# Performance work log

Hardware: AMD Instinct MI355X
Metric: run time of the kernel (lower is better)

The kernel has to match this reference:

```python
import jax, jax.numpy as jnp
import numpy as np

N = 50000      # nodes
E = 800000     # edges (avg degree 16)
F_IN = 256
F_OUT = 128
ALPHA = 0.2    # leaky-relu negative slope


def setup_inputs() -> dict:
    key = jax.random.key(0)
    k1, k2, k3, k4 = jax.random.split(key, 4)
    x = jax.random.normal(k1, (N, F_IN), dtype=jnp.float32)
    # xavier_uniform-like scale for W (gain=1.414)
    limit_w = 1.414 * np.sqrt(6.0 / (F_IN + F_OUT))
    W = jax.random.uniform(k2, (F_IN, F_OUT), dtype=jnp.float32, minval=-limit_w, maxval=limit_w)
    limit_a = 1.414 * np.sqrt(6.0 / (2 * F_OUT + 1))
    a = jax.random.uniform(k3, (2 * F_OUT, 1), dtype=jnp.float32, minval=-limit_a, maxval=limit_a)
    edge = jax.random.randint(k4, (2, E), 0, N)  # edge[0]=row/src, edge[1]=col/dst
    return {"x": x, "W": W, "a": a, "edge": edge}


def reference(x, W, a, edge):
    h = x @ W                                   # [N, F_OUT]
    src, dst = edge[0], edge[1]                 # [E], [E]
    # cat([h_i, h_j], 1) @ a == h_i @ a[:F] + h_j @ a[F:] -> compute per-node halves once
    s_src = h @ a[:F_OUT, 0]                    # [N]
    s_dst = h @ a[F_OUT:, 0]                    # [N]
    e = jax.nn.leaky_relu(s_src[src] + s_dst[dst], negative_slope=ALPHA)  # [E]
    # segment softmax over edges grouped by row (dim=1 softmax of sparse [N,N])
    m = jax.ops.segment_max(e, src, num_segments=N)       # [N], -inf for empty rows
    ex = jnp.exp(e - m[src])                               # [E]
    denom = jax.ops.segment_sum(ex, src, num_segments=N)   # [N]
    attn = ex / denom[src]                                  # [E]
    # sparse mm: h_prime[i] = sum_{edges with row i} attn * h[dst]
    h_prime = jax.ops.segment_sum(attn[:, None] * h[dst], src, num_segments=N)  # [N, F_OUT]
    return jax.nn.elu(h_prime)                  # concat=True path
```

## Files before the change

kernel.cpp:

```cpp
#include <hip/hip_runtime.h>
#include <hip/hip_bf16.h>
#include <math.h>

#define F_IN   256
#define F_OUT  128
#define ALPHA  0.2f
#define TM     64

typedef __attribute__((ext_vector_type(8))) short s16x8;
typedef __attribute__((ext_vector_type(4))) float f32x4;

__device__ __forceinline__ ushort f2bf(float f) {
  __hip_bfloat16 h = __float2bfloat16(f);
  return *reinterpret_cast<ushort*>(&h);
}
__device__ __forceinline__ uint pk2bf(float lo, float hi) {
  return (uint)f2bf(lo) | ((uint)f2bf(hi) << 16);
}
__device__ __forceinline__ float bflo(uint u) { return __uint_as_float(u << 16); }
__device__ __forceinline__ float bfhi(uint u) { return __uint_as_float(u & 0xffff0000u); }

__global__ __launch_bounds__(256) void prep_kernel(
    const float* __restrict__ W, const float* __restrict__ avec,
    ushort* __restrict__ Wf, ushort* __restrict__ Wfs,
    int4* __restrict__ deg4, int n4, int ZB) {
  int b = blockIdx.x;
  if (b < ZB) {
    int i = b * 256 + threadIdx.x;
    if (i < n4) deg4[i] = make_int4(0, 0, 0, 0);
  } else if (b < ZB + 16) {
    int idx = (b - ZB) * 256 + threadIdx.x;
    int kb = idx >> 7, c = idx & 127;
    union { s16x8 v; ushort u[8]; } t;
#pragma unroll
    for (int j = 0; j < 8; ++j) t.u[j] = f2bf(W[(kb * 8 + j) * F_OUT + c]);
    *(s16x8*)&Wf[(size_t)idx * 8] = t.v;
  } else {
    int k = threadIdx.x;
    float s1 = 0.f, s2 = 0.f;
    for (int c = 0; c < F_OUT; ++c) {
      float wv = W[k * F_OUT + c];
      s1 += wv * avec[c];
      s2 += wv * avec[F_OUT + c];
    }
    int kb = k >> 3, j8 = k & 7;
    ushort b1 = f2bf(s1), b2 = f2bf(s2);
#pragma unroll
    for (int cc = 0; cc < 16; ++cc) {
      ushort v = (cc == 0) ? b1 : (cc == 1) ? b2 : (ushort)0;
      Wfs[((size_t)kb * 16 + cc) * 8 + j8] = v;
    }
  }
}

__global__ __launch_bounds__(256) void gemm_hist_kernel(
    const float* __restrict__ X, const ushort* __restrict__ Wf,
    const ushort* __restrict__ Wfs,
    uint* __restrict__ Hb32, float* __restrict__ s_src, float* __restrict__ s_dst,
    int M, int G,
    const int* __restrict__ src, int* __restrict__ deg,
    int* __restrict__ rank, int E) {
  __shared__ __align__(16) char Xs[TM * 256 * 2];
  const int tid = threadIdx.x;

  if (blockIdx.x >= G) {
    int e0 = ((blockIdx.x - G) * 256 + tid) * 4;
    if (e0 + 4 <= E) {
      int4 s4 = *(const int4*)(src + e0);
      int4 r4;
      r4.x = atomicAdd(&deg[s4.x], 1);
      r4.y = atomicAdd(&deg[s4.y], 1);
      r4.z = atomicAdd(&deg[s4.z], 1);
      r4.w = atomicAdd(&deg[s4.w], 1);
      *(int4*)(rank + e0) = r4;
    } else {
      for (int e = e0; e < E; ++e) rank[e] = atomicAdd(&deg[src[e]], 1);
    }
    return;
  }

  const int l = tid & 63;
  const int w = tid >> 6;
  const int lc = l & 15;
  const int lg = l >> 4;
  const int row0 = blockIdx.x * TM;

  s16x8 bfr0[8], bfr1[8];
#pragma unroll
  for (int ks = 0; ks < 8; ++ks) {
    int kb = ks * 4 + lg;
    bfr0[ks] = *(const s16x8*)&Wf[((size_t)kb * F_OUT + w * 16 + lc) * 8];
    bfr1[ks] = *(const s16x8*)&Wf[((size_t)kb * F_OUT + 64 + w * 16 + lc) * 8];
  }

#pragma unroll
  for (int half = 0; half < 2; ++half) {
    f32x4 v[8];
#pragma unroll
    for (int u = 0; u < 4; ++u) {
      int idx = (half * 4 + u) * 256 + tid;
      int r = idx >> 5, kb = idx & 31;
      int gr = row0 + r; gr = (gr < M) ? gr : (M - 1);
      const f32x4* p = (const f32x4*)&X[(size_t)gr * F_IN + kb * 8];
      v[u * 2]     = p[0];
      v[u * 2 + 1] = p[1];
    }
#pragma unroll
    for (int u = 0; u < 4; ++u) {
      int idx = (half * 4 + u) * 256 + tid;
      int r = idx >> 5, kb = idx & 31;
      f32x4 v0 = v[u * 2], v1 = v[u * 2 + 1];
      union { s16x8 vv; ushort uu[8]; } t;
      t.uu[0] = f2bf(v0[0]); t.uu[1] = f2bf(v0[1]); t.uu[2] = f2bf(v0[2]); t.uu[3] = f2bf(v0[3]);
      t.uu[4] = f2bf(v1[0]); t.uu[5] = f2bf(v1[1]); t.uu[6] = f2bf(v1[2]); t.uu[7] = f2bf(v1[3]);
      int byte = ((r >> 4) * 8192) + kb * 256 + (r & 15) * 16;
      byte ^= (kb & 7) << 4;
      *(s16x8*)(Xs + byte) = t.vv;
    }
  }
  __syncthreads();

  f32x4 acc0[4] = {}, acc1[4] = {}, accS[4] = {};
#pragma unroll
  for (int ks = 0; ks < 8; ++ks) {
    int kb = ks * 4 + lg;
    int ab = kb * 256 + lc * 16;
    ab ^= (kb & 7) << 4;
    s16x8 bS;
    if (w == 0) bS = *(const s16x8*)&Wfs[((size_t)kb * 16 + lc) * 8];
#pragma unroll
    for (int rf = 0; rf < 4; ++rf) {
      s16x8 af = *(const s16x8*)(Xs + rf * 8192 + ab);
      acc0[rf] = __builtin_amdgcn_mfma_f32_16x16x32_bf16(af, bfr0[ks], acc0[rf], 0, 0, 0);
      acc1[rf] = __builtin_amdgcn_mfma_f32_16x16x32_bf16(af, bfr1[ks], acc1[rf], 0, 0, 0);
      if (w == 0)
        accS[rf] = __builtin_amdgcn_mfma_f32_16x16x32_bf16(af, bS, accS[rf], 0, 0, 0);
    }
  }

#pragma unroll
  for (int rf = 0; rf < 4; ++rf) {
#pragma unroll
    for (int q = 0; q < 4; ++q) {
      int rg = row0 + rf * 16 + lg * 4 + q;
      if (rg < M)
        Hb32[(size_t)rg * 64 + w * 16 + lc] = pk2bf(acc0[rf][q], acc1[rf][q]);
    }
  }

  if (w == 0 && lc < 2) {
    float* sout = (lc == 0) ? s_src : s_dst;
#pragma unroll
    for (int rf = 0; rf < 4; ++rf) {
#pragma unroll
      for (int q = 0; q < 4; ++q) {
        int rg = row0 + rf * 16 + lg * 4 + q;
        if (rg < M) sout[rg] = accS[rf][q];
      }
    }
  }
}

__global__ void block_sums_kernel(const int* __restrict__ deg, int* __restrict__ bs, int N) {
  int i = blockIdx.x * 256 + threadIdx.x;
  int v = (i < N) ? deg[i] : 0;
  int lane = threadIdx.x & 63, w = threadIdx.x >> 6;
#pragma unroll
  for (int d = 32; d >= 1; d >>= 1) v += __shfl_down(v, d);
  __shared__ int wsum[4];
  if (lane == 0) wsum[w] = v;
  __syncthreads();
  if (threadIdx.x == 0) bs[blockIdx.x] = wsum[0] + wsum[1] + wsum[2] + wsum[3];
}

__global__ void scan_deg_kernel(const int* __restrict__ deg, const int* __restrict__ bs,
                                int* __restrict__ rowptr, int N, int E, int NS) {
  __shared__ int sc[256];
  __shared__ int wsumA[4], wsumB[4];
  int tid = threadIdx.x;
  int lane = tid & 63, w = tid >> 6;

  int bv = (tid < NS) ? bs[tid] : 0;
  int ibv = bv;
#pragma unroll
  for (int d = 1; d < 64; d <<= 1) {
    int t = __shfl_up(ibv, d);
    if (lane >= d) ibv += t;
  }
  if (lane == 63) wsumA[w] = ibv;
  __syncthreads();
  int boff = 0;
  for (int x = 0; x < w; ++x) boff += wsumA[x];
  sc[tid] = boff + ibv - bv;

  int i = blockIdx.x * 256 + tid;
  int v = (i < N) ? deg[i] : 0;
  int iv = v;
#pragma unroll
  for (int d = 1; d < 64; d <<= 1) {
    int t = __shfl_up(iv, d);
    if (lane >= d) iv += t;
  }
  if (lane == 63) wsumB[w] = iv;
  __syncthreads();
  int off = sc[blockIdx.x];
  for (int x = 0; x < w; ++x) off += wsumB[x];
  int excl = off + iv - v;
  if (i < N) rowptr[i] = excl;
  if (i == N - 1) rowptr[N] = E;
}

__global__ __launch_bounds__(256) void scatter_kernel(
    const int* __restrict__ src, const int* __restrict__ dst,
    const int* __restrict__ rank, const int* __restrict__ rowptr,
    int* __restrict__ colidx, int E) {
  int e0 = (blockIdx.x * 256 + threadIdx.x) * 4;
  if (e0 + 4 <= E) {
    int4 s4 = *(const int4*)(src + e0);
    int4 d4 = *(const int4*)(dst + e0);
    int4 r4 = *(const int4*)(rank + e0);
    colidx[rowptr[s4.x] + r4.x] = d4.x;
    colidx[rowptr[s4.y] + r4.y] = d4.y;
    colidx[rowptr[s4.z] + r4.z] = d4.z;
    colidx[rowptr[s4.w] + r4.w] = d4.w;
  } else {
    for (int e = e0; e < E; ++e) colidx[rowptr[src[e]] + rank[e]] = dst[e];
  }
}

__global__ __launch_bounds__(256) void aggregate_kernel(
    const uint* __restrict__ H32, const float* __restrict__ s_src,
    const float* __restrict__ s_dst, const int* __restrict__ rowptr,
    const int* __restrict__ colidx, float* __restrict__ out, int M) {
  int node = blockIdx.x * 4 + (threadIdx.x >> 6);
  int l = threadIdx.x & 63;
  if (node >= M) return;
  const int g = l >> 4;
  const int lc = l & 15;
  int beg = rowptr[node], end = rowptr[node + 1];
  float ssrc = s_src[node];
  float m = -INFINITY, denom = 0.f;
  float acc[8] = {};

  for (int base = beg; base < end; base += 64) {
    int cnt = end - base; if (cnt > 64) cnt = 64;
    int jv = 0; float ev = -INFINITY;
    if (l < cnt) {
      jv = colidx[base + l];
      float e = ssrc + s_dst[jv];
      ev = (e > 0.f) ? e : ALPHA * e;
    }
    float cm = ev;
#pragma unroll
    for (int mask = 1; mask < 64; mask <<= 1) cm = fmaxf(cm, __shfl_xor(cm, mask));
    float mn = fmaxf(m, cm);
    float wv = (l < cnt) ? __expf(ev - mn) : 0.f;
    float sw = wv;
#pragma unroll
    for (int mask = 1; mask < 64; mask <<= 1) sw += __shfl_xor(sw, mask);
    float resc = __expf(m - mn);
    denom = denom * resc + sw;
#pragma unroll
    for (int t = 0; t < 8; ++t) acc[t] *= resc;
    m = mn;

    for (int k = 0; k < cnt; k += 8) {
      int k0 = k + g, k1 = k + 4 + g;
      int j0 = __shfl(jv, k0);
      int j1 = (k1 < 64) ? __shfl(jv, k1) : 0;
      float w0 = __shfl(wv, k0);
      float w1 = (k1 < 64) ? __shfl(wv, k1) : 0.f;
      uint4 u0 = *(const uint4*)(H32 + ((size_t)(uint)j0 << 6) + lc * 4);
      uint4 u1 = *(const uint4*)(H32 + ((size_t)(uint)j1 << 6) + lc * 4);
      acc[0] += w0 * bflo(u0.x) + w1 * bflo(u1.x);
      acc[1] += w0 * bfhi(u0.x) + w1 * bfhi(u1.x);
      acc[2] += w0 * bflo(u0.y) + w1 * bflo(u1.y);
      acc[3] += w0 * bfhi(u0.y) + w1 * bfhi(u1.y);
      acc[4] += w0 * bflo(u0.z) + w1 * bflo(u1.z);
      acc[5] += w0 * bfhi(u0.z) + w1 * bfhi(u1.z);
      acc[6] += w0 * bflo(u0.w) + w1 * bflo(u1.w);
      acc[7] += w0 * bfhi(u0.w) + w1 * bfhi(u1.w);
    }
  }

#pragma unroll
  for (int t = 0; t < 8; ++t) {
    acc[t] += __shfl_xor(acc[t], 16);
    acc[t] += __shfl_xor(acc[t], 32);
  }
  float inv = (denom > 0.f) ? 1.f / denom : 0.f;
  if (g == 0) {
    float4 v;
    v.x = acc[0] * inv; v.y = acc[2] * inv; v.z = acc[4] * inv; v.w = acc[6] * inv;
    v.x = (v.x > 0.f) ? v.x : __expf(v.x) - 1.f;
    v.y = (v.y > 0.f) ? v.y : __expf(v.y) - 1.f;
    v.z = (v.z > 0.f) ? v.z : __expf(v.z) - 1.f;
    v.w = (v.w > 0.f) ? v.w : __expf(v.w) - 1.f;
    *(float4*)&out[(size_t)node * 128 + lc * 4] = v;
  } else if (g == 1) {
    float4 v;
    v.x = acc[1] * inv; v.y = acc[3] * inv; v.z = acc[5] * inv; v.w = acc[7] * inv;
    v.x = (v.x > 0.f) ? v.x : __expf(v.x) - 1.f;
    v.y = (v.y > 0.f) ? v.y : __expf(v.y) - 1.f;
    v.z = (v.z > 0.f) ? v.z : __expf(v.z) - 1.f;
    v.w = (v.w > 0.f) ? v.w : __expf(v.w) - 1.f;
    *(float4*)&out[(size_t)node * 128 + 64 + lc * 4] = v;
  }
}

extern "C" void kernel_launch(void* const* d_in, const int* in_sizes, int n_in,
                              void* d_out, int out_size, void* d_ws, size_t ws_size,
                              hipStream_t stream) {
  const float* x    = (const float*)d_in[0];
  const float* W    = (const float*)d_in[1];
  const float* avec = (const float*)d_in[2];
  const int*   edge = (const int*)d_in[3];

  const int M = in_sizes[0] / F_IN;
  const int E = in_sizes[3] / 2;
  const int* src = edge;
  const int* dst = edge + E;
  float* out = (float*)d_out;

  char* ws = (char*)d_ws;
  uint*   Hb32  = (uint*)ws;   ws += (size_t)M * 64 * sizeof(uint);
  ushort* Wf    = (ushort*)ws; ws += (size_t)32 * F_OUT * 8 * sizeof(ushort);
  ushort* Wfs   = (ushort*)ws; ws += (size_t)32 * 16 * 8 * sizeof(ushort);
  float* s_src  = (float*)ws;  ws += (size_t)M * sizeof(float);
  float* s_dst  = (float*)ws;  ws += (size_t)M * sizeof(float);
  int*   deg    = (int*)ws;    ws += (size_t)M * sizeof(int);
  int*   rowptr = (int*)ws;    ws += (size_t)(M + 1) * sizeof(int);
  int*   rank   = (int*)ws;    ws += (size_t)E * sizeof(int);
  int*   colidx = (int*)ws;    ws += (size_t)E * sizeof(int);
  int*   bsums  = (int*)ws;

  const int NS = (M + 255) / 256;
  const int n4 = M / 4;
  const int ZB = (n4 + 255) / 256;
  const int E4 = (E + 1023) / 1024;
  const int G  = (M + TM - 1) / TM;

  prep_kernel<<<ZB + 17, 256, 0, stream>>>(W, avec, Wf, Wfs, (int4*)deg, n4, ZB);
  gemm_hist_kernel<<<G + E4, 256, 0, stream>>>(x, Wf, Wfs, Hb32, s_src, s_dst,
                                               M, G, src, deg, rank, E);
  block_sums_kernel<<<NS, 256, 0, stream>>>(deg, bsums, M);
  scan_deg_kernel<<<NS, 256, 0, stream>>>(deg, bsums, rowptr, M, E, NS);
  scatter_kernel<<<E4, 256, 0, stream>>>(src, dst, rank, rowptr, colidx, E);
  aggregate_kernel<<<(M + 3) / 4, 256, 0, stream>>>(Hb32, s_src, s_dst, rowptr, colidx, out, M);
}
```

Baseline: 111.7 us.

## Split histogram from GEMM and load X fragments directly into registers

The fused GEMM+histogram launch is split into two kernels, a standalone degree-histogram/rank kernel and a GEMM kernel. The GEMM no longer stages X through LDS with a swizzled layout and a barrier. Each wave now loads its own X rows straight from global memory into MFMA fragment registers and converts them to bf16 inline, and W fragments are loaded per k-step instead of preloaded. This removes LDS traffic and the block barrier, but each of the four waves reloads the same X tile from global/L2 (4x redundant reads) and loses the overlap between the histogram atomics and the GEMM in one grid.

```diff
diff --git a/kernel.cpp b/kernel.cpp
--- a/kernel.cpp
+++ b/kernel.cpp
@@ -53,88 +53,53 @@
   }
 }
 
-__global__ __launch_bounds__(256) void gemm_hist_kernel(
+__global__ __launch_bounds__(256) void gemm_mfma_kernel(
     const float* __restrict__ X, const ushort* __restrict__ Wf,
     const ushort* __restrict__ Wfs,
     uint* __restrict__ Hb32, float* __restrict__ s_src, float* __restrict__ s_dst,
-    int M, int G,
-    const int* __restrict__ src, int* __restrict__ deg,
-    int* __restrict__ rank, int E) {
-  __shared__ __align__(16) char Xs[TM * 256 * 2];
+    int M) {
   const int tid = threadIdx.x;
-
-  if (blockIdx.x >= G) {
-    int e0 = ((blockIdx.x - G) * 256 + tid) * 4;
-    if (e0 + 4 <= E) {
-      int4 s4 = *(const int4*)(src + e0);
-      int4 r4;
-      r4.x = atomicAdd(&deg[s4.x], 1);
-      r4.y = atomicAdd(&deg[s4.y], 1);
-      r4.z = atomicAdd(&deg[s4.z], 1);
-      r4.w = atomicAdd(&deg[s4.w], 1);
-      *(int4*)(rank + e0) = r4;
-    } else {
-      for (int e = e0; e < E; ++e) rank[e] = atomicAdd(&deg[src[e]], 1);
-    }
-    return;
-  }
-
   const int l = tid & 63;
   const int w = tid >> 6;
   const int lc = l & 15;
   const int lg = l >> 4;
   const int row0 = blockIdx.x * TM;
 
-  s16x8 bfr0[8], bfr1[8];
+  const float* xp[4];
+#pragma unroll
+  for (int rf = 0; rf < 4; ++rf) {
+    int gr = row0 + rf * 16 + lc;
+    gr = (gr < M) ? gr : (M - 1);
+    xp[rf] = X + (size_t)gr * F_IN + lg * 8;
+  }
+
+  f32x4 acc0[4] = {}, acc1[4] = {}, accS[4] = {};
 #pragma unroll
   for (int ks = 0; ks < 8; ++ks) {
+    f32x4 ra[4][2];
+#pragma unroll
+    for (int rf = 0; rf < 4; ++rf) {
+      const f32x4* p = (const f32x4*)(xp[rf] + ks * 32);
+      ra[rf][0] = p[0];
+      ra[rf][1] = p[1];
+    }
     int kb = ks * 4 + lg;
-    bfr0[ks] = *(const s16x8*)&Wf[((size_t)kb * F_OUT + w * 16 + lc) * 8];
-    bfr1[ks] = *(const s16x8*)&Wf[((size_t)kb * F_OUT + 64 + w * 16 + lc) * 8];
-  }
-
-#pragma unroll
-  for (int half = 0; half < 2; ++half) {
-    f32x4 v[8];
-#pragma unroll
-    for (int u = 0; u < 4; ++u) {
-      int idx = (half * 4 + u) * 256 + tid;
-      int r = idx >> 5, kb = idx & 31;
-      int gr = row0 + r; gr = (gr < M) ? gr : (M - 1);
-      const f32x4* p = (const f32x4*)&X[(size_t)gr * F_IN + kb * 8];
-      v[u * 2]     = p[0];
-      v[u * 2 + 1] = p[1];
-    }
-#pragma unroll
-    for (int u = 0; u < 4; ++u) {
-      int idx = (half * 4 + u) * 256 + tid;
-      int r = idx >> 5, kb = idx & 31;
-      f32x4 v0 = v[u * 2], v1 = v[u * 2 + 1];
-      union { s16x8 vv; ushort uu[8]; } t;
-      t.uu[0] = f2bf(v0[0]); t.uu[1] = f2bf(v0[1]); t.uu[2] = f2bf(v0[2]); t.uu[3] = f2bf(v0[3]);
-      t.uu[4] = f2bf(v1[0]); t.uu[5] = f2bf(v1[1]); t.uu[6] = f2bf(v1[2]); t.uu[7] = f2bf(v1[3]);
-      int byte = ((r >> 4) * 8192) + kb * 256 + (r & 15) * 16;
-      byte ^= (kb & 7) << 4;
-      *(s16x8*)(Xs + byte) = t.vv;
-    }
-  }
-  __syncthreads();
-
-  f32x4 acc0[4] = {}, acc1[4] = {}, accS[4] = {};
-#pragma unroll
-  for (int ks = 0; ks < 8; ++ks) {
-    int kb = ks * 4 + lg;
-    int ab = kb * 256 + lc * 16;
-    ab ^= (kb & 7) << 4;
+    s16x8 b0 = *(const s16x8*)&Wf[((size_t)kb * F_OUT + w * 16 + lc) * 8];
+    s16x8 b1 = *(const s16x8*)&Wf[((size_t)kb * F_OUT + 64 + w * 16 + lc) * 8];
     s16x8 bS;
     if (w == 0) bS = *(const s16x8*)&Wfs[((size_t)kb * 16 + lc) * 8];
+
 #pragma unroll
     for (int rf = 0; rf < 4; ++rf) {
-      s16x8 af = *(const s16x8*)(Xs + rf * 8192 + ab);
-      acc0[rf] = __builtin_amdgcn_mfma_f32_16x16x32_bf16(af, bfr0[ks], acc0[rf], 0, 0, 0);
-      acc1[rf] = __builtin_amdgcn_mfma_f32_16x16x32_bf16(af, bfr1[ks], acc1[rf], 0, 0, 0);
+      union { s16x8 v; ushort u[8]; } t;
+      t.u[0] = f2bf(ra[rf][0][0]); t.u[1] = f2bf(ra[rf][0][1]);
+      t.u[2] = f2bf(ra[rf][0][2]); t.u[3] = f2bf(ra[rf][0][3]);
+      t.u[4] = f2bf(ra[rf][1][0]); t.u[5] = f2bf(ra[rf][1][1]);
+      t.u[6] = f2bf(ra[rf][1][2]); t.u[7] = f2bf(ra[rf][1][3]);
+      acc0[rf] = __builtin_amdgcn_mfma_f32_16x16x32_bf16(t.v, b0, acc0[rf], 0, 0, 0);
+      acc1[rf] = __builtin_amdgcn_mfma_f32_16x16x32_bf16(t.v, b1, acc1[rf], 0, 0, 0);
       if (w == 0)
-        accS[rf] = __builtin_amdgcn_mfma_f32_16x16x32_bf16(af, bS, accS[rf], 0, 0, 0);
+        accS[rf] = __builtin_amdgcn_mfma_f32_16x16x32_bf16(t.v, bS, accS[rf], 0, 0, 0);
     }
   }
 
@@ -158,6 +123,23 @@
         if (rg < M) sout[rg] = accS[rf][q];
       }
     }
+  }
+}
+
+__global__ __launch_bounds__(256) void hist_rank_kernel(
+    const int* __restrict__ src, int* __restrict__ deg,
+    int* __restrict__ rank, int E) {
+  int e0 = (blockIdx.x * 256 + threadIdx.x) * 4;
+  if (e0 + 4 <= E) {
+    int4 s4 = *(const int4*)(src + e0);
+    int4 r4;
+    r4.x = atomicAdd(&deg[s4.x], 1);
+    r4.y = atomicAdd(&deg[s4.y], 1);
+    r4.z = atomicAdd(&deg[s4.z], 1);
+    r4.w = atomicAdd(&deg[s4.w], 1);
+    *(int4*)(rank + e0) = r4;
+  } else {
+    for (int e = e0; e < E; ++e) rank[e] = atomicAdd(&deg[src[e]], 1);
   }
 }
 
@@ -341,8 +323,8 @@
   const int G  = (M + TM - 1) / TM;
 
   prep_kernel<<<ZB + 17, 256, 0, stream>>>(W, avec, Wf, Wfs, (int4*)deg, n4, ZB);
-  gemm_hist_kernel<<<G + E4, 256, 0, stream>>>(x, Wf, Wfs, Hb32, s_src, s_dst,
-                                               M, G, src, deg, rank, E);
+  hist_rank_kernel<<<E4, 256, 0, stream>>>(src, deg, rank, E);
+  gemm_mfma_kernel<<<G, 256, 0, stream>>>(x, Wf, Wfs, Hb32, s_src, s_dst, M);
   block_sums_kernel<<<NS, 256, 0, stream>>>(deg, bsums, M);
   scan_deg_kernel<<<NS, 256, 0, stream>>>(deg, bsums, rowptr, M, E, NS);
   scatter_kernel<<<E4, 256, 0, stream>>>(src, dst, rank, rowptr, colidx, E);
```

Result: slower. 134.0 us (+19.9%).
